# Optimization experiments

Measured on AMD Instinct MI355X. Metric: run time of the kernel, lower is better.

Reference implementation:

```python
import jax, jax.numpy as jnp
import numpy as np

N, Q, D = 8, 900, 256
HB, WB = 200, 200
L, NH, P = 6, 8, 4
HD = D // NH
FF = 512
NCLS, NBOX = 10, 8
ODIM = NCLS + NBOX
THRESH = 0.5
OFFSET_SCALE = 1.0
SCALE = 1.0 / float(np.sqrt(HD))


def _ln(x, g, b, eps=1e-5):
    m = jnp.mean(x, axis=-1, keepdims=True)
    v = jnp.mean((x - m) ** 2, axis=-1, keepdims=True)
    return (x - m) * jax.lax.rsqrt(v + eps) * g + b


def _mha(x, Wq, bq, Wk, bk, Wv, bv, Wo, bo):
    q = (x @ Wq + bq).reshape(N, Q, NH, HD)
    k = (x @ Wk + bk).reshape(N, Q, NH, HD)
    v = (x @ Wv + bv).reshape(N, Q, NH, HD)
    att = jax.nn.softmax(jnp.einsum('bqhd,bkhd->bhqk', q, k) * SCALE, axis=-1)
    o = jnp.einsum('bhqk,bkhd->bqhd', att, v).reshape(N, Q, D)
    return o @ Wo + bo


def _deform(q, ref, bev, dv_W, dv_b, off_W, off_b, aw_W, aw_b, do_W, do_b):
    # value projection of BEV map: (N, HW, D) -> (N, NH, HW, HD)
    val = (bev @ dv_W + dv_b).reshape(N, HB * WB, NH, HD).transpose(0, 2, 1, 3)
    off = (q @ off_W + off_b).reshape(N, Q, NH, P, 2)
    aw = jax.nn.softmax((q @ aw_W + aw_b).reshape(N, Q, NH, P), axis=-1)
    # ref: (N,Q,1,2) pixel coords -> broadcast to (N,Q,NH,P,2)
    loc = ref[:, :, :, None, :] + off * OFFSET_SCALE
    x = jnp.clip(loc[..., 0], 0.0, WB - 1.0)
    y = jnp.clip(loc[..., 1], 0.0, HB - 1.0)
    x0 = jnp.floor(x)
    y0 = jnp.floor(y)
    x1 = jnp.minimum(x0 + 1.0, WB - 1.0)
    y1 = jnp.minimum(y0 + 1.0, HB - 1.0)
    wx = (x - x0).transpose(0, 2, 1, 3)[..., None]  # (N,NH,Q,P,1)
    wy = (y - y0).transpose(0, 2, 1, 3)[..., None]

    def gather(ix, iy):
        idx = (iy * WB + ix).astype(jnp.int32)               # (N,Q,NH,P)
        idx = idx.transpose(0, 2, 1, 3).reshape(N, NH, Q * P, 1)
        g = jnp.take_along_axis(val, idx, axis=2)            # (N,NH,Q*P,HD)
        return g.reshape(N, NH, Q, P, HD)

    samp = (gather(x0, y0) * (1 - wx) * (1 - wy)
            + gather(x1, y0) * wx * (1 - wy)
            + gather(x0, y1) * (1 - wx) * wy
            + gather(x1, y1) * wx * wy)                      # (N,NH,Q,P,HD)
    awt = aw.transpose(0, 2, 1, 3)                           # (N,NH,Q,P)
    out = jnp.einsum('bhqp,bhqpd->bqhd', awt, samp).reshape(N, Q, D)
    return out @ do_W + do_b


def _ref_points():
    # n_sample=Q points evenly spread over the HBxWB grid, pixel coords, unnormalized
    idx = jnp.round(jnp.linspace(0.0, HB * WB - 1.0, Q)).astype(jnp.int32)
    x = (idx % WB).astype(jnp.float32)
    y = (idx // WB).astype(jnp.float32)
    rp = jnp.stack([x, y], axis=-1)                          # (Q,2)
    return jnp.broadcast_to(rp[None, :, None, :], (N, Q, 1, 2))


def _det(x, W1, b1, W2, b2):
    h = jax.nn.relu(x @ W1 + b1)
    o = h @ W2 + b2
    return jnp.concatenate([jax.nn.sigmoid(o[..., :NCLS]), o[..., NCLS:]], axis=-1)


def setup_inputs() -> dict:
    key = jax.random.key(0)
    ks = iter(jax.random.split(key, 48))

    def w(shape, s=0.02):
        return jax.random.normal(next(ks), shape, jnp.float32) * s

    inp = {
        'bev_features': jax.random.normal(next(ks), (N, HB * WB, D), jnp.float32),
        'pos_emb': w((Q, D), 1.0),
        'Wq': w((L, D, D)), 'bq': jnp.zeros((L, D), jnp.float32),
        'Wk': w((L, D, D)), 'bk': jnp.zeros((L, D), jnp.float32),
        'Wv': w((L, D, D)), 'bv': jnp.zeros((L, D), jnp.float32),
        'Wo': w((L, D, D)), 'bo': jnp.zeros((L, D), jnp.float32),
        'ln1_g': jnp.ones((L, D), jnp.float32), 'ln1_b': jnp.zeros((L, D), jnp.float32),
        'ln2_g': jnp.ones((L, D), jnp.float32), 'ln2_b': jnp.zeros((L, D), jnp.float32),
        'ln3_g': jnp.ones((L, D), jnp.float32), 'ln3_b': jnp.zeros((L, D), jnp.float32),
        'dv_W': w((L, D, D)), 'dv_b': jnp.zeros((L, D), jnp.float32),
        'off_W': w((L, D, NH * P * 2), 0.01), 'off_b': jnp.zeros((L, NH * P * 2), jnp.float32),
        'aw_W': w((L, D, NH * P), 0.01), 'aw_b': jnp.zeros((L, NH * P), jnp.float32),
        'do_W': w((L, D, D)), 'do_b': jnp.zeros((L, D), jnp.float32),
        'f1_W': w((L, D, FF)), 'f1_b': jnp.zeros((L, FF), jnp.float32),
        'f2_W': w((L, FF, D)), 'f2_b': jnp.zeros((L, D), jnp.float32),
        'det_W1': w((D, D)), 'det_b1': jnp.zeros((D,), jnp.float32),
        'det_W2': w((D, ODIM)), 'det_b2': jnp.zeros((ODIM,), jnp.float32),
    }
    return inp


def reference(bev_features, pos_emb, Wq, bq, Wk, bk, Wv, bv, Wo, bo,
              ln1_g, ln1_b, ln2_g, ln2_b, ln3_g, ln3_b,
              dv_W, dv_b, off_W, off_b, aw_W, aw_b, do_W, do_b,
              f1_W, f1_b, f2_W, f2_b, det_W1, det_b1, det_W2, det_b2):
    queries = jnp.broadcast_to(pos_emb[None], (N, Q, D))
    ref = _ref_points()
    output = queries
    layer_results = []
    for i in range(L):
        x = output + queries
        a = _mha(x, Wq[i], bq[i], Wk[i], bk[i], Wv[i], bv[i], Wo[i], bo[i])
        x2 = _ln(x + a, ln1_g[i], ln1_b[i])
        d = _deform(x2, ref, bev_features, dv_W[i], dv_b[i], off_W[i], off_b[i],
                    aw_W[i], aw_b[i], do_W[i], do_b[i])
        x3 = _ln(x2 + d, ln2_g[i], ln2_b[i])
        f = jax.nn.relu(x3 @ f1_W[i] + f1_b[i]) @ f2_W[i] + f2_b[i]
        output = _ln(x3 + f, ln3_g[i], ln3_b[i])
        layer_results.append(_det(output, det_W1, det_b1, det_W2, det_b2))
    layer_results = jnp.stack(layer_results, axis=0)   # (L,N,Q,ODIM)
    detections = layer_results[-1]
    track_mask = detections[..., 0] >= THRESH
    return output, detections, track_mask, layer_results
```

## Files before the change

kernel.cpp:

```cpp
#include <hip/hip_runtime.h>
#include <hip/hip_bf16.h>
#include <math.h>

#define N 8
#define Q 900
#define D 256
#define HB 200
#define WB 200
#define L 6
#define NH 8
#define P 4
#define HD 32
#define FF 512
#define NCLS 10
#define ODIM 18
#define HW (HB*WB)
#define NQ (N*Q)
#define NQD (NQ*D)
#define QD (Q*D)
#define SCALE 0.17677669529663687f

typedef __attribute__((ext_vector_type(4))) float f32x4;
typedef __attribute__((ext_vector_type(8))) short short8v;

__device__ __forceinline__ short bf16_of(float f) {
  __hip_bfloat16 h = __float2bfloat16(f);
  return __builtin_bit_cast(short, h);
}

#define TM 64
#define TN 64
#define KC 128

template <int ACT>
__global__ __launch_bounds__(256) void gemm_kernel(
    const float* __restrict__ A, const float* __restrict__ B,
    const float* __restrict__ bias, float* __restrict__ C,
    int M, int K, int Nc) {
  __shared__ float AsT[KC][TM + 4];
  __shared__ float Bs[KC][TN + 4];
  const int tid = threadIdx.x;
  const int tx = tid & 15, ty = tid >> 4;
  const int m0 = blockIdx.x * TM, n0 = blockIdx.y * TN;

  float c[4][4] = {};

  for (int kc = 0; kc < K; kc += KC) {
    {
      int r = tid >> 2;
      int gr = m0 + r;
      int kb = (tid & 3) * 32;
#pragma unroll
      for (int q = 0; q < 8; ++q) {
        int k = kb + q * 4;
        float4 av = make_float4(0.f, 0.f, 0.f, 0.f);
        if (gr < M) av = *(const float4*)(A + (size_t)gr * K + kc + k);
        AsT[k + 0][r] = av.x; AsT[k + 1][r] = av.y;
        AsT[k + 2][r] = av.z; AsT[k + 3][r] = av.w;
      }
    }
    {
#pragma unroll
      for (int i = 0; i < 8; ++i) {
        int idx = i * 256 + tid;
        int kr = idx >> 4;
        int c4 = (idx & 15) * 4;
        *(float4*)&Bs[kr][c4] = *(const float4*)(B + (size_t)(kc + kr) * Nc + n0 + c4);
      }
    }
    __syncthreads();
#pragma unroll 8
    for (int kk = 0; kk < KC; ++kk) {
      float4 av = *(const float4*)&AsT[kk][ty * 4];
      float4 bv = *(const float4*)&Bs[kk][tx * 4];
      c[0][0] += av.x * bv.x; c[0][1] += av.x * bv.y; c[0][2] += av.x * bv.z; c[0][3] += av.x * bv.w;
      c[1][0] += av.y * bv.x; c[1][1] += av.y * bv.y; c[1][2] += av.y * bv.z; c[1][3] += av.y * bv.w;
      c[2][0] += av.z * bv.x; c[2][1] += av.z * bv.y; c[2][2] += av.z * bv.z; c[2][3] += av.z * bv.w;
      c[3][0] += av.w * bv.x; c[3][1] += av.w * bv.y; c[3][2] += av.w * bv.z; c[3][3] += av.w * bv.w;
    }
    __syncthreads();
  }

#pragma unroll
  for (int i = 0; i < 4; ++i) {
    int row = m0 + ty * 4 + i;
    if (row >= M) continue;
#pragma unroll
    for (int j = 0; j < 4; ++j) {
      int col = n0 + tx * 4 + j;
      float v = c[i][j] + bias[col];
      if (ACT == 1) v = fmaxf(v, 0.f);
      C[(size_t)row * Nc + col] = v;
    }
  }
}

__global__ __launch_bounds__(256) void gemm_qkv_kernel(
    const float* __restrict__ outp, const float* __restrict__ pos,
    const float* __restrict__ Wq, const float* __restrict__ bq,
    const float* __restrict__ Wk, const float* __restrict__ bk,
    const float* __restrict__ Wv, const float* __restrict__ bv,
    float* __restrict__ Oq, float* __restrict__ Ok, float* __restrict__ Ov) {
  __shared__ float AsT[KC][TM + 4];
  __shared__ float Bs[KC][TN + 4];
  const int tid = threadIdx.x;
  const int tx = tid & 15, ty = tid >> 4;
  const int m0 = blockIdx.x * TM;
  const int wsel = blockIdx.y >> 2;
  const int n0 = (blockIdx.y & 3) * TN;
  const float* B = (wsel == 0) ? Wq : (wsel == 1) ? Wk : Wv;
  const float* bias = (wsel == 0) ? bq : (wsel == 1) ? bk : bv;
  float* C = (wsel == 0) ? Oq : (wsel == 1) ? Ok : Ov;

  float c[4][4] = {};

  for (int kc = 0; kc < D; kc += KC) {
    {
      int r = tid >> 2;
      int gr = m0 + r;
      int kb = (tid & 3) * 32;
      const float* ar = outp + (size_t)gr * D + kc;
      const float* pr = pos + (size_t)(gr % Q) * D + kc;
#pragma unroll
      for (int q = 0; q < 8; ++q) {
        int k = kb + q * 4;
        float4 av = make_float4(0.f, 0.f, 0.f, 0.f);
        if (gr < NQ) {
          float4 ov = *(const float4*)(ar + k);
          float4 pv = *(const float4*)(pr + k);
          av.x = ov.x + pv.x; av.y = ov.y + pv.y; av.z = ov.z + pv.z; av.w = ov.w + pv.w;
        }
        AsT[k + 0][r] = av.x; AsT[k + 1][r] = av.y;
        AsT[k + 2][r] = av.z; AsT[k + 3][r] = av.w;
      }
    }
    {
#pragma unroll
      for (int i = 0; i < 8; ++i) {
        int idx = i * 256 + tid;
        int kr = idx >> 4;
        int c4 = (idx & 15) * 4;
        *(float4*)&Bs[kr][c4] = *(const float4*)(B + (size_t)(kc + kr) * D + n0 + c4);
      }
    }
    __syncthreads();
#pragma unroll 8
    for (int kk = 0; kk < KC; ++kk) {
      float4 av = *(const float4*)&AsT[kk][ty * 4];
      float4 bv4 = *(const float4*)&Bs[kk][tx * 4];
      c[0][0] += av.x * bv4.x; c[0][1] += av.x * bv4.y; c[0][2] += av.x * bv4.z; c[0][3] += av.x * bv4.w;
      c[1][0] += av.y * bv4.x; c[1][1] += av.y * bv4.y; c[1][2] += av.y * bv4.z; c[1][3] += av.y * bv4.w;
      c[2][0] += av.z * bv4.x; c[2][1] += av.z * bv4.y; c[2][2] += av.z * bv4.z; c[2][3] += av.z * bv4.w;
      c[3][0] += av.w * bv4.x; c[3][1] += av.w * bv4.y; c[3][2] += av.w * bv4.z; c[3][3] += av.w * bv4.w;
    }
    __syncthreads();
  }

#pragma unroll
  for (int i = 0; i < 4; ++i) {
    int row = m0 + ty * 4 + i;
    if (row >= NQ) continue;
#pragma unroll
    for (int j = 0; j < 4; ++j) {
      int col = n0 + tx * 4 + j;
      C[(size_t)row * D + col] = c[i][j] + bias[col];
    }
  }
}

#define TMT 64
#define TKT 16
template <int ACT>
__global__ __launch_bounds__(256) void gemm_thin_kernel(
    const float* __restrict__ A, const float* __restrict__ B,
    const float* __restrict__ bias, float* __restrict__ C,
    int M, int K, int Nc) {
  __shared__ float AsT[TKT][TMT + 4];
  __shared__ float Bs[TKT][16 + 2];
  const int tid = threadIdx.x;
  const int tx = tid & 15, ty = tid >> 4;
  const int m0 = blockIdx.x * TMT, n0 = blockIdx.y * 16;

  float c[4] = {};

  for (int kt = 0; kt < K; kt += TKT) {
    {
      int r = tid >> 2;
      int cb = (tid & 3) * 4;
      int gr = m0 + r;
      float4 av = make_float4(0.f, 0.f, 0.f, 0.f);
      if (gr < M) av = *(const float4*)(A + (size_t)gr * K + kt + cb);
      AsT[cb + 0][r] = av.x;
      AsT[cb + 1][r] = av.y;
      AsT[cb + 2][r] = av.z;
      AsT[cb + 3][r] = av.w;
    }
    {
      int r = tid >> 4;
      int cc = tid & 15;
      int gc = n0 + cc;
      Bs[r][cc] = (gc < Nc) ? B[(size_t)(kt + r) * Nc + gc] : 0.f;
    }
    __syncthreads();
#pragma unroll
    for (int kk = 0; kk < TKT; ++kk) {
      float4 av = *(const float4*)&AsT[kk][ty * 4];
      float bv = Bs[kk][tx];
      c[0] += av.x * bv; c[1] += av.y * bv; c[2] += av.z * bv; c[3] += av.w * bv;
    }
    __syncthreads();
  }

  int col = n0 + tx;
  if (col < Nc) {
    float bs = bias[col];
#pragma unroll
    for (int i = 0; i < 4; ++i) {
      int row = m0 + ty * 4 + i;
      if (row < M) {
        float v = c[i] + bs;
        if (ACT == 2 && col < NCLS) v = 1.f / (1.f + expf(-v));
        C[(size_t)row * Nc + col] = v;
      }
    }
  }
}

__global__ __launch_bounds__(256) void gemm_offaw_kernel(
    const float* __restrict__ A,
    const float* __restrict__ offW, const float* __restrict__ offb,
    const float* __restrict__ awW, const float* __restrict__ awb,
    float* __restrict__ offC, float* __restrict__ awC) {
  __shared__ float AsT[TKT][TMT + 4];
  __shared__ float Bs[TKT][16 + 2];
  const int tid = threadIdx.x;
  const int tx = tid & 15, ty = tid >> 4;
  const int m0 = blockIdx.x * TMT;
  const bool isOff = blockIdx.y < 4;
  const int n0 = isOff ? blockIdx.y * 16 : (blockIdx.y - 4) * 16;
  const int Nc = isOff ? 64 : 32;
  const float* B = isOff ? offW : awW;
  const float* bias = isOff ? offb : awb;
  float* C = isOff ? offC : awC;

  float c[4] = {};

  for (int kt = 0; kt < D; kt += TKT) {
    {
      int r = tid >> 2;
      int cb = (tid & 3) * 4;
      int gr = m0 + r;
      float4 av = make_float4(0.f, 0.f, 0.f, 0.f);
      if (gr < NQ) av = *(const float4*)(A + (size_t)gr * D + kt + cb);
      AsT[cb + 0][r] = av.x;
      AsT[cb + 1][r] = av.y;
      AsT[cb + 2][r] = av.z;
      AsT[cb + 3][r] = av.w;
    }
    {
      int r = tid >> 4;
      int cc = tid & 15;
      Bs[r][cc] = B[(size_t)(kt + r) * Nc + n0 + cc];
    }
    __syncthreads();
#pragma unroll
    for (int kk = 0; kk < TKT; ++kk) {
      float4 av = *(const float4*)&AsT[kk][ty * 4];
      float bv = Bs[kk][tx];
      c[0] += av.x * bv; c[1] += av.y * bv; c[2] += av.z * bv; c[3] += av.w * bv;
    }
    __syncthreads();
  }

  int col = n0 + tx;
  float bs = bias[col];
#pragma unroll
  for (int i = 0; i < 4; ++i) {
    int row = m0 + ty * 4 + i;
    if (row < NQ) C[(size_t)row * Nc + col] = c[i] + bs;
  }
}

__global__ __launch_bounds__(256) void attn_kernel(
    const float* __restrict__ qg, const float* __restrict__ kg,
    const float* __restrict__ vg, float* __restrict__ og) {
  const int n = blockIdx.z, h = blockIdx.y;
  const int wv = threadIdx.x >> 6;
  const int lane = threadIdx.x & 63;
  const int g = lane >> 4;
  const int c = lane & 15;
  const int q0 = blockIdx.x * 64 + wv * 16;

  const float* qb = qg + (size_t)n * Q * D + h * HD;
  const float* kb = kg + (size_t)n * Q * D + h * HD;
  const float* vb = vg + (size_t)n * Q * D + h * HD;

  short8v qf = {};
  {
    int qr = q0 + c;
    if (qr < Q) {
      const float* qp = qb + (size_t)qr * D + g * 8;
#pragma unroll
      for (int j = 0; j < 8; ++j) qf[j] = bf16_of(qp[j]);
    }
  }

  const float SC2 = SCALE * 1.4426950408889634f;
  float m2 = -1e30f, l = 0.f;
  f32x4 acc0 = {0.f, 0.f, 0.f, 0.f}, acc1 = {0.f, 0.f, 0.f, 0.f};

  for (int kt0 = 0; kt0 < Q; kt0 += 64) {
    float s[16];
#pragma unroll
    for (int t = 0; t < 4; ++t) {
      short8v kf = {};
      int kr = kt0 + t * 16 + c;
      if (kr < Q) {
        const float* kp = kb + (size_t)kr * D + g * 8;
#pragma unroll
        for (int j = 0; j < 8; ++j) kf[j] = bf16_of(kp[j]);
      }
      f32x4 d = __builtin_amdgcn_mfma_f32_16x16x32_bf16(kf, qf, (f32x4){0.f, 0.f, 0.f, 0.f}, 0, 0, 0);
#pragma unroll
      for (int r = 0; r < 4; ++r) s[t * 4 + r] = d[r];
    }
#pragma unroll
    for (int t = 0; t < 4; ++t)
#pragma unroll
      for (int r = 0; r < 4; ++r) {
        int key = kt0 + t * 16 + g * 4 + r;
        s[t * 4 + r] = (key < Q) ? s[t * 4 + r] * SC2 : -1e30f;
      }
    float tm = s[0];
#pragma unroll
    for (int j = 1; j < 16; ++j) tm = fmaxf(tm, s[j]);
    tm = fmaxf(tm, __shfl_xor(tm, 16));
    tm = fmaxf(tm, __shfl_xor(tm, 32));
    float m2n = fmaxf(m2, tm);
    float corr = exp2f(m2 - m2n);
    m2 = m2n;
    float ps = 0.f;
#pragma unroll
    for (int j = 0; j < 16; ++j) { s[j] = exp2f(s[j] - m2); ps += s[j]; }
    ps += __shfl_xor(ps, 16);
    ps += __shfl_xor(ps, 32);
    l = l * corr + ps;
    float cr0 = __shfl(corr, g * 4 + 0);
    float cr1 = __shfl(corr, g * 4 + 1);
    float cr2 = __shfl(corr, g * 4 + 2);
    float cr3 = __shfl(corr, g * 4 + 3);
    acc0[0] *= cr0; acc0[1] *= cr1; acc0[2] *= cr2; acc0[3] *= cr3;
    acc1[0] *= cr0; acc1[1] *= cr1; acc1[2] *= cr2; acc1[3] *= cr3;

#pragma unroll
    for (int pr = 0; pr < 2; ++pr) {
      short8v pa, v0 = {}, v1 = {};
#pragma unroll
      for (int j = 0; j < 8; ++j) pa[j] = bf16_of(s[pr * 8 + j]);
#pragma unroll
      for (int j = 0; j < 8; ++j) {
        int key = kt0 + (pr * 2 + (j >> 2)) * 16 + g * 4 + (j & 3);
        if (key < Q) {
          const float* vp = vb + (size_t)key * D;
          v0[j] = bf16_of(vp[c]);
          v1[j] = bf16_of(vp[c + 16]);
        }
      }
      acc0 = __builtin_amdgcn_mfma_f32_16x16x32_bf16(pa, v0, acc0, 0, 0, 0);
      acc1 = __builtin_amdgcn_mfma_f32_16x16x32_bf16(pa, v1, acc1, 0, 0, 0);
    }
  }

  float inv = 1.f / l;
  float iv[4];
#pragma unroll
  for (int r = 0; r < 4; ++r) iv[r] = __shfl(inv, g * 4 + r);
#pragma unroll
  for (int r = 0; r < 4; ++r) {
    int qr = q0 + g * 4 + r;
    if (qr < Q) {
      float* op = og + (size_t)(n * Q + qr) * D + h * HD;
      op[c] = acc0[r] * iv[r];
      op[c + 16] = acc1[r] * iv[r];
    }
  }
}

__global__ __launch_bounds__(256) void ln_add_kernel(
    const float* __restrict__ A, const float* __restrict__ Bp,
    const float* __restrict__ g, const float* __restrict__ b,
    float* __restrict__ out) {
  const int wave = threadIdx.x >> 6;
  const int lane = threadIdx.x & 63;
  const int row = blockIdx.x * 4 + wave;
  const size_t base = (size_t)row * D + lane * 4;
  float4 a4 = *(const float4*)(A + base);
  float4 b4 = *(const float4*)(Bp + base);
  float v0 = a4.x + b4.x, v1 = a4.y + b4.y, v2 = a4.z + b4.z, v3 = a4.w + b4.w;
  float sum = v0 + v1 + v2 + v3;
#pragma unroll
  for (int off = 1; off < 64; off <<= 1) sum += __shfl_xor(sum, off);
  float mean = sum * (1.f / D);
  float d0 = v0 - mean, d1 = v1 - mean, d2 = v2 - mean, d3 = v3 - mean;
  float vsum = d0 * d0 + d1 * d1 + d2 * d2 + d3 * d3;
#pragma unroll
  for (int off = 1; off < 64; off <<= 1) vsum += __shfl_xor(vsum, off);
  float inv_std = 1.0f / sqrtf(vsum * (1.f / D) + 1e-5f);
  float4 g4 = *(const float4*)(g + lane * 4);
  float4 bb4 = *(const float4*)(b + lane * 4);
  float4 o4;
  o4.x = d0 * inv_std * g4.x + bb4.x;
  o4.y = d1 * inv_std * g4.y + bb4.y;
  o4.z = d2 * inv_std * g4.z + bb4.z;
  o4.w = d3 * inv_std * g4.w + bb4.w;
  *(float4*)(out + base) = o4;
}

__global__ __launch_bounds__(256) void ln_add3_kernel(
    const float* __restrict__ A, const float* __restrict__ pos,
    const float* __restrict__ Bp,
    const float* __restrict__ g, const float* __restrict__ b,
    float* __restrict__ out) {
  const int wave = threadIdx.x >> 6;
  const int lane = threadIdx.x & 63;
  const int row = blockIdx.x * 4 + wave;
  const size_t base = (size_t)row * D + lane * 4;
  const size_t pbase = (size_t)(row % Q) * D + lane * 4;
  float4 a4 = *(const float4*)(A + base);
  float4 p4 = *(const float4*)(pos + pbase);
  float4 b4 = *(const float4*)(Bp + base);
  float x0 = a4.x + p4.x, x1 = a4.y + p4.y, x2 = a4.z + p4.z, x3 = a4.w + p4.w;
  float v0 = x0 + b4.x, v1 = x1 + b4.y, v2 = x2 + b4.z, v3 = x3 + b4.w;
  float sum = v0 + v1 + v2 + v3;
#pragma unroll
  for (int off = 1; off < 64; off <<= 1) sum += __shfl_xor(sum, off);
  float mean = sum * (1.f / D);
  float d0 = v0 - mean, d1 = v1 - mean, d2 = v2 - mean, d3 = v3 - mean;
  float vsum = d0 * d0 + d1 * d1 + d2 * d2 + d3 * d3;
#pragma unroll
  for (int off = 1; off < 64; off <<= 1) vsum += __shfl_xor(vsum, off);
  float inv_std = 1.0f / sqrtf(vsum * (1.f / D) + 1e-5f);
  float4 g4 = *(const float4*)(g + lane * 4);
  float4 bb4 = *(const float4*)(b + lane * 4);
  float4 o4;
  o4.x = d0 * inv_std * g4.x + bb4.x;
  o4.y = d1 * inv_std * g4.y + bb4.y;
  o4.z = d2 * inv_std * g4.z + bb4.z;
  o4.w = d3 * inv_std * g4.w + bb4.w;
  *(float4*)(out + base) = o4;
}

__global__ __launch_bounds__(256) void deform_kernel(
    const float* __restrict__ bev, const float* __restrict__ offB,
    const float* __restrict__ awB, const float* __restrict__ dvW,
    const float* __restrict__ dvb, float* __restrict__ dtmp) {
  const int bq0 = blockIdx.x * 4;
  const int n = bq0 / Q;
  const int t = threadIdx.x;

  __shared__ float aw_s[4][NH * P];
  __shared__ int   idx_s[4][NH * P * 4];
  __shared__ float w_s[4][NH * P * 4];
  __shared__ float agg_s[4][NH][D];
  __shared__ float red_s[4][4][D];

  if (t < 128) {
    int qq = t >> 5, e = t & 31;
    int bq = bq0 + qq;
    int qi = bq - n * Q;
    float tq = __fmul_rn((float)qi, 44.492767333984375f);
    int ir = (int)rintf(tq);
    float rx = (float)(ir % WB);
    float ry = (float)(ir / WB);
    float ox = offB[(size_t)bq * 64 + e * 2 + 0];
    float oy = offB[(size_t)bq * 64 + e * 2 + 1];
    float lx = fminf(fmaxf(rx + ox, 0.f), (float)(WB - 1));
    float ly = fminf(fmaxf(ry + oy, 0.f), (float)(HB - 1));
    float x0 = floorf(lx), y0 = floorf(ly);
    float x1 = fminf(x0 + 1.f, (float)(WB - 1));
    float y1 = fminf(y0 + 1.f, (float)(HB - 1));
    float wx = lx - x0, wy = ly - y0;
    int b4 = e * 4;
    idx_s[qq][b4 + 0] = (int)y0 * WB + (int)x0; w_s[qq][b4 + 0] = (1.f - wx) * (1.f - wy);
    idx_s[qq][b4 + 1] = (int)y0 * WB + (int)x1; w_s[qq][b4 + 1] = wx * (1.f - wy);
    idx_s[qq][b4 + 2] = (int)y1 * WB + (int)x0; w_s[qq][b4 + 2] = (1.f - wx) * wy;
    idx_s[qq][b4 + 3] = (int)y1 * WB + (int)x1; w_s[qq][b4 + 3] = wx * wy;
  } else if (t < 160) {
    int idx = t - 128;
    int qq = idx >> 3, hh = idx & 7;
    const float* ap = awB + (size_t)(bq0 + qq) * 32 + hh * P;
    float l0 = ap[0], l1 = ap[1], l2 = ap[2], l3 = ap[3];
    float mx = fmaxf(fmaxf(l0, l1), fmaxf(l2, l3));
    float e0 = expf(l0 - mx), e1 = expf(l1 - mx), e2 = expf(l2 - mx), e3 = expf(l3 - mx);
    float inv = 1.f / (e0 + e1 + e2 + e3);
    aw_s[qq][hh * P + 0] = e0 * inv; aw_s[qq][hh * P + 1] = e1 * inv;
    aw_s[qq][hh * P + 2] = e2 * inv; aw_s[qq][hh * P + 3] = e3 * inv;
  }
  __syncthreads();

  {
    const float* bevn = bev + (size_t)n * HW * D;
    const int wv = t >> 6, lane = t & 63;
    const int c4 = lane * 4;
#pragma unroll
    for (int u = 0; u < 8; ++u) {
      int pid = wv + u * 4;
      int qq = pid >> 3, h = pid & 7;
      f32x4 acc = {0.f, 0.f, 0.f, 0.f};
#pragma unroll
      for (int p = 0; p < P; ++p) {
        int e = h * P + p;
        float aw = aw_s[qq][e];
        const int* ix = &idx_s[qq][e * 4];
        const float* wsp = &w_s[qq][e * 4];
        float4 g0 = *(const float4*)(bevn + (size_t)ix[0] * D + c4);
        float4 g1 = *(const float4*)(bevn + (size_t)ix[1] * D + c4);
        float4 g2 = *(const float4*)(bevn + (size_t)ix[2] * D + c4);
        float4 g3 = *(const float4*)(bevn + (size_t)ix[3] * D + c4);
        acc[0] += aw * (wsp[0] * g0.x + wsp[1] * g1.x + wsp[2] * g2.x + wsp[3] * g3.x);
        acc[1] += aw * (wsp[0] * g0.y + wsp[1] * g1.y + wsp[2] * g2.y + wsp[3] * g3.y);
        acc[2] += aw * (wsp[0] * g0.z + wsp[1] * g1.z + wsp[2] * g2.z + wsp[3] * g3.z);
        acc[3] += aw * (wsp[0] * g0.w + wsp[1] * g1.w + wsp[2] * g2.w + wsp[3] * g3.w);
      }
      *(f32x4*)&agg_s[qq][h][c4] = acc;
    }
  }
  __syncthreads();

  {
    const int chunk = t >> 6;
    const int col4 = t & 63;
    const int tt0 = col4 * 4;
    const int h = tt0 >> 5;
    f32x4 p[4] = {{0.f,0.f,0.f,0.f},{0.f,0.f,0.f,0.f},{0.f,0.f,0.f,0.f},{0.f,0.f,0.f,0.f}};
#pragma unroll 4
    for (int dd4 = 0; dd4 < 64; dd4 += 4) {
      int dd = chunk * 64 + dd4;
      float4 w0 = *(const float4*)(dvW + (size_t)(dd + 0) * D + tt0);
      float4 w1 = *(const float4*)(dvW + (size_t)(dd + 1) * D + tt0);
      float4 w2 = *(const float4*)(dvW + (size_t)(dd + 2) * D + tt0);
      float4 w3 = *(const float4*)(dvW + (size_t)(dd + 3) * D + tt0);
#pragma unroll
      for (int qq = 0; qq < 4; ++qq) {
        float4 a = *(const float4*)&agg_s[qq][h][dd];
        p[qq][0] += a.x * w0.x + a.y * w1.x + a.z * w2.x + a.w * w3.x;
        p[qq][1] += a.x * w0.y + a.y * w1.y + a.z * w2.y + a.w * w3.y;
        p[qq][2] += a.x * w0.z + a.y * w1.z + a.z * w2.z + a.w * w3.z;
        p[qq][3] += a.x * w0.w + a.y * w1.w + a.z * w2.w + a.w * w3.w;
      }
    }
#pragma unroll
    for (int qq = 0; qq < 4; ++qq) *(f32x4*)&red_s[qq][chunk][tt0] = p[qq];
  }
  __syncthreads();
  {
    float bs = dvb[t];
#pragma unroll
    for (int qq = 0; qq < 4; ++qq) {
      dtmp[(size_t)(bq0 + qq) * D + t] =
          bs + red_s[qq][0][t] + red_s[qq][1][t] + red_s[qq][2][t] + red_s[qq][3][t];
    }
  }
}

__global__ void bcast_q_kernel(const float* __restrict__ pos, float* __restrict__ out) {
  for (size_t i = (size_t)blockIdx.x * blockDim.x + threadIdx.x; i < (size_t)NQD;
       i += (size_t)gridDim.x * blockDim.x)
    out[i] = pos[i % QD];
}
__global__ void finalize_kernel(const float* __restrict__ lr5, float* __restrict__ det,
                                float* __restrict__ mask) {
  int i = blockIdx.x * blockDim.x + threadIdx.x;
  if (i < NQ * ODIM) det[i] = lr5[i];
  if (i < NQ) mask[i] = (lr5[(size_t)i * ODIM] >= 0.5f) ? 1.0f : 0.0f;
}

extern "C" void kernel_launch(void* const* d_in, const int* in_sizes, int n_in,
                              void* d_out, int out_size, void* d_ws, size_t ws_size,
                              hipStream_t stream) {
  const float* bev  = (const float*)d_in[0];
  const float* pos  = (const float*)d_in[1];
  const float* Wq   = (const float*)d_in[2];  const float* bq  = (const float*)d_in[3];
  const float* Wk   = (const float*)d_in[4];  const float* bk  = (const float*)d_in[5];
  const float* Wv   = (const float*)d_in[6];  const float* bv  = (const float*)d_in[7];
  const float* Wo   = (const float*)d_in[8];  const float* bo  = (const float*)d_in[9];
  const float* ln1g = (const float*)d_in[10]; const float* ln1b = (const float*)d_in[11];
  const float* ln2g = (const float*)d_in[12]; const float* ln2b = (const float*)d_in[13];
  const float* ln3g = (const float*)d_in[14]; const float* ln3b = (const float*)d_in[15];
  const float* dvW  = (const float*)d_in[16]; const float* dvb = (const float*)d_in[17];
  const float* offW = (const float*)d_in[18]; const float* offb = (const float*)d_in[19];
  const float* awW  = (const float*)d_in[20]; const float* awb = (const float*)d_in[21];
  const float* doW  = (const float*)d_in[22]; const float* dob = (const float*)d_in[23];
  const float* f1W  = (const float*)d_in[24]; const float* f1b = (const float*)d_in[25];
  const float* f2W  = (const float*)d_in[26]; const float* f2b = (const float*)d_in[27];
  const float* dW1  = (const float*)d_in[28]; const float* db1 = (const float*)d_in[29];
  const float* dW2  = (const float*)d_in[30]; const float* db2 = (const float*)d_in[31];

  float* w = (float*)d_ws;
  float* b0 = w + 0 * (size_t)NQD;
  float* b1 = w + 1 * (size_t)NQD;
  float* b2 = w + 2 * (size_t)NQD;
  float* b3 = w + 3 * (size_t)NQD;
  float* ffh = b1;
  float* offB = b0;
  float* awB  = b0 + (size_t)NQ * 64;

  float* out_output = (float*)d_out;
  float* out_det    = out_output + (size_t)NQD;
  float* out_mask   = out_det + (size_t)NQ * ODIM;
  float* out_lr     = out_mask + (size_t)NQ;

  const dim3 blk256(256);
  const dim3 qkvGrid((NQ + TM - 1) / TM, 12);
  const dim3 gemmGridD((NQ + TM - 1) / TM, D / TN);
  const dim3 gemmGridFF((NQ + TM - 1) / TM, FF / TN);
  const dim3 offawGrid((NQ + TMT - 1) / TMT, 6);
  const dim3 thinGridDet((NQ + TMT - 1) / TMT, 2);
  const dim3 attnGrid((Q + 63) / 64, NH, N);
  const dim3 lnGrid(NQ / 4);
  const dim3 defGrid(NQ / 4);
  const int ewGrid = 1024;

  bcast_q_kernel<<<ewGrid, blk256, 0, stream>>>(pos, out_output);

  for (int i = 0; i < L; ++i) {
    const size_t wDD = (size_t)i * D * D;
    gemm_qkv_kernel<<<qkvGrid, blk256, 0, stream>>>(out_output, pos,
        Wq + wDD, bq + (size_t)i * D, Wk + wDD, bk + (size_t)i * D,
        Wv + wDD, bv + (size_t)i * D, b1, b2, b3);
    attn_kernel<<<attnGrid, blk256, 0, stream>>>(b1, b2, b3, b0);
    gemm_kernel<0><<<gemmGridD, blk256, 0, stream>>>(b0, Wo + wDD, bo + (size_t)i * D, b1, NQ, D, D);
    ln_add3_kernel<<<lnGrid, blk256, 0, stream>>>(out_output, pos, b1,
        ln1g + (size_t)i * D, ln1b + (size_t)i * D, b2);
    gemm_offaw_kernel<<<offawGrid, blk256, 0, stream>>>(b2,
        offW + (size_t)i * D * 64, offb + (size_t)i * 64,
        awW + (size_t)i * D * 32, awb + (size_t)i * 32, offB, awB);
    deform_kernel<<<defGrid, blk256, 0, stream>>>(bev, offB, awB, dvW + wDD, dvb + (size_t)i * D, b3);
    gemm_kernel<0><<<gemmGridD, blk256, 0, stream>>>(b3, doW + wDD, dob + (size_t)i * D, b1, NQ, D, D);
    ln_add_kernel<<<lnGrid, blk256, 0, stream>>>(b2, b1, ln2g + (size_t)i * D, ln2b + (size_t)i * D, b0);
    gemm_kernel<1><<<gemmGridFF, blk256, 0, stream>>>(b0, f1W + (size_t)i * D * FF, f1b + (size_t)i * FF, ffh, NQ, D, FF);
    gemm_kernel<0><<<gemmGridD, blk256, 0, stream>>>(ffh, f2W + (size_t)i * FF * D, f2b + (size_t)i * D, b3, NQ, FF, D);
    ln_add_kernel<<<lnGrid, blk256, 0, stream>>>(b0, b3, ln3g + (size_t)i * D, ln3b + (size_t)i * D, out_output);
    gemm_kernel<1><<<gemmGridD, blk256, 0, stream>>>(out_output, dW1, db1, b1, NQ, D, D);
    gemm_thin_kernel<2><<<thinGridDet, blk256, 0, stream>>>(b1, dW2, db2, out_lr + (size_t)i * NQ * ODIM, NQ, D, ODIM);
  }

  finalize_kernel<<<(NQ * ODIM + 255) / 256, blk256, 0, stream>>>(out_lr + (size_t)(L - 1) * NQ * ODIM,
                                                                  out_det, out_mask);
}
```

Before: 2.522 ms.

## Store QKV projections as bf16 and enlarge K-chunk in thin GEMMs

```diff
diff --git a/kernel.cpp b/kernel.cpp
--- a/kernel.cpp
+++ b/kernel.cpp
@@ -100,7 +100,8 @@
     const float* __restrict__ Wq, const float* __restrict__ bq,
     const float* __restrict__ Wk, const float* __restrict__ bk,
     const float* __restrict__ Wv, const float* __restrict__ bv,
-    float* __restrict__ Oq, float* __restrict__ Ok, float* __restrict__ Ov) {
+    unsigned short* __restrict__ Oq, unsigned short* __restrict__ Ok,
+    unsigned short* __restrict__ Ov) {
   __shared__ float AsT[KC][TM + 4];
   __shared__ float Bs[KC][TN + 4];
   const int tid = threadIdx.x;
@@ -110,7 +111,7 @@
   const int n0 = (blockIdx.y & 3) * TN;
   const float* B = (wsel == 0) ? Wq : (wsel == 1) ? Wk : Wv;
   const float* bias = (wsel == 0) ? bq : (wsel == 1) ? bk : bv;
-  float* C = (wsel == 0) ? Oq : (wsel == 1) ? Ok : Ov;
+  unsigned short* C = (wsel == 0) ? Oq : (wsel == 1) ? Ok : Ov;
 
   float c[4][4] = {};
 
@@ -160,50 +161,56 @@
   for (int i = 0; i < 4; ++i) {
     int row = m0 + ty * 4 + i;
     if (row >= NQ) continue;
-#pragma unroll
-    for (int j = 0; j < 4; ++j) {
-      int col = n0 + tx * 4 + j;
-      C[(size_t)row * D + col] = c[i][j] + bias[col];
-    }
+    ushort4 o4;
+    o4.x = (unsigned short)bf16_of(c[i][0] + bias[n0 + tx * 4 + 0]);
+    o4.y = (unsigned short)bf16_of(c[i][1] + bias[n0 + tx * 4 + 1]);
+    o4.z = (unsigned short)bf16_of(c[i][2] + bias[n0 + tx * 4 + 2]);
+    o4.w = (unsigned short)bf16_of(c[i][3] + bias[n0 + tx * 4 + 3]);
+    *(ushort4*)(C + (size_t)row * D + n0 + tx * 4) = o4;
   }
 }
 
 #define TMT 64
-#define TKT 16
 template <int ACT>
 __global__ __launch_bounds__(256) void gemm_thin_kernel(
     const float* __restrict__ A, const float* __restrict__ B,
     const float* __restrict__ bias, float* __restrict__ C,
     int M, int K, int Nc) {
-  __shared__ float AsT[TKT][TMT + 4];
-  __shared__ float Bs[TKT][16 + 2];
+  __shared__ float AsT[KC][TMT + 4];
+  __shared__ float Bs[KC][16 + 2];
   const int tid = threadIdx.x;
   const int tx = tid & 15, ty = tid >> 4;
   const int m0 = blockIdx.x * TMT, n0 = blockIdx.y * 16;
 
   float c[4] = {};
 
-  for (int kt = 0; kt < K; kt += TKT) {
+  for (int kc = 0; kc < K; kc += KC) {
     {
       int r = tid >> 2;
-      int cb = (tid & 3) * 4;
       int gr = m0 + r;
-      float4 av = make_float4(0.f, 0.f, 0.f, 0.f);
-      if (gr < M) av = *(const float4*)(A + (size_t)gr * K + kt + cb);
-      AsT[cb + 0][r] = av.x;
-      AsT[cb + 1][r] = av.y;
-      AsT[cb + 2][r] = av.z;
-      AsT[cb + 3][r] = av.w;
-    }
-    {
-      int r = tid >> 4;
-      int cc = tid & 15;
-      int gc = n0 + cc;
-      Bs[r][cc] = (gc < Nc) ? B[(size_t)(kt + r) * Nc + gc] : 0.f;
-    }
-    __syncthreads();
-#pragma unroll
-    for (int kk = 0; kk < TKT; ++kk) {
+      int kb = (tid & 3) * 32;
+#pragma unroll
+      for (int q = 0; q < 8; ++q) {
+        int k = kb + q * 4;
+        float4 av = make_float4(0.f, 0.f, 0.f, 0.f);
+        if (gr < M) av = *(const float4*)(A + (size_t)gr * K + kc + k);
+        AsT[k + 0][r] = av.x; AsT[k + 1][r] = av.y;
+        AsT[k + 2][r] = av.z; AsT[k + 3][r] = av.w;
+      }
+    }
+    {
+#pragma unroll
+      for (int i = 0; i < 8; ++i) {
+        int idx = i * 256 + tid;
+        int kr = idx >> 4;
+        int cc = idx & 15;
+        int gc = n0 + cc;
+        Bs[kr][cc] = (gc < Nc) ? B[(size_t)(kc + kr) * Nc + gc] : 0.f;
+      }
+    }
+    __syncthreads();
+#pragma unroll 8
+    for (int kk = 0; kk < KC; ++kk) {
       float4 av = *(const float4*)&AsT[kk][ty * 4];
       float bv = Bs[kk][tx];
       c[0] += av.x * bv; c[1] += av.y * bv; c[2] += av.z * bv; c[3] += av.w * bv;
@@ -231,8 +238,8 @@
     const float* __restrict__ offW, const float* __restrict__ offb,
     const float* __restrict__ awW, const float* __restrict__ awb,
     float* __restrict__ offC, float* __restrict__ awC) {
-  __shared__ float AsT[TKT][TMT + 4];
-  __shared__ float Bs[TKT][16 + 2];
+  __shared__ float AsT[KC][TMT + 4];
+  __shared__ float Bs[KC][16 + 2];
   const int tid = threadIdx.x;
   const int tx = tid & 15, ty = tid >> 4;
   const int m0 = blockIdx.x * TMT;
@@ -245,26 +252,32 @@
 
   float c[4] = {};
 
-  for (int kt = 0; kt < D; kt += TKT) {
+  for (int kc = 0; kc < D; kc += KC) {
     {
       int r = tid >> 2;
-      int cb = (tid & 3) * 4;
       int gr = m0 + r;
-      float4 av = make_float4(0.f, 0.f, 0.f, 0.f);
-      if (gr < NQ) av = *(const float4*)(A + (size_t)gr * D + kt + cb);
-      AsT[cb + 0][r] = av.x;
-      AsT[cb + 1][r] = av.y;
-      AsT[cb + 2][r] = av.z;
-      AsT[cb + 3][r] = av.w;
-    }
-    {
-      int r = tid >> 4;
-      int cc = tid & 15;
-      Bs[r][cc] = B[(size_t)(kt + r) * Nc + n0 + cc];
-    }
-    __syncthreads();
-#pragma unroll
-    for (int kk = 0; kk < TKT; ++kk) {
+      int kb = (tid & 3) * 32;
+#pragma unroll
+      for (int q = 0; q < 8; ++q) {
+        int k = kb + q * 4;
+        float4 av = make_float4(0.f, 0.f, 0.f, 0.f);
+        if (gr < NQ) av = *(const float4*)(A + (size_t)gr * D + kc + k);
+        AsT[k + 0][r] = av.x; AsT[k + 1][r] = av.y;
+        AsT[k + 2][r] = av.z; AsT[k + 3][r] = av.w;
+      }
+    }
+    {
+#pragma unroll
+      for (int i = 0; i < 8; ++i) {
+        int idx = i * 256 + tid;
+        int kr = idx >> 4;
+        int cc = idx & 15;
+        Bs[kr][cc] = B[(size_t)(kc + kr) * Nc + n0 + cc];
+      }
+    }
+    __syncthreads();
+#pragma unroll 8
+    for (int kk = 0; kk < KC; ++kk) {
       float4 av = *(const float4*)&AsT[kk][ty * 4];
       float bv = Bs[kk][tx];
       c[0] += av.x * bv; c[1] += av.y * bv; c[2] += av.z * bv; c[3] += av.w * bv;
@@ -282,8 +295,8 @@
 }
 
 __global__ __launch_bounds__(256) void attn_kernel(
-    const float* __restrict__ qg, const float* __restrict__ kg,
-    const float* __restrict__ vg, float* __restrict__ og) {
+    const unsigned short* __restrict__ qg, const unsigned short* __restrict__ kg,
+    const unsigned short* __restrict__ vg, float* __restrict__ og) {
   const int n = blockIdx.z, h = blockIdx.y;
   const int wv = threadIdx.x >> 6;
   const int lane = threadIdx.x & 63;
@@ -291,18 +304,14 @@
   const int c = lane & 15;
   const int q0 = blockIdx.x * 64 + wv * 16;
 
-  const float* qb = qg + (size_t)n * Q * D + h * HD;
-  const float* kb = kg + (size_t)n * Q * D + h * HD;
-  const float* vb = vg + (size_t)n * Q * D + h * HD;
+  const unsigned short* qb = qg + (size_t)n * Q * D + h * HD;
+  const unsigned short* kb = kg + (size_t)n * Q * D + h * HD;
+  const unsigned short* vb = vg + (size_t)n * Q * D + h * HD;
 
   short8v qf = {};
   {
     int qr = q0 + c;
-    if (qr < Q) {
-      const float* qp = qb + (size_t)qr * D + g * 8;
-#pragma unroll
-      for (int j = 0; j < 8; ++j) qf[j] = bf16_of(qp[j]);
-    }
+    if (qr < Q) qf = *(const short8v*)(qb + (size_t)qr * D + g * 8);
   }
 
   const float SC2 = SCALE * 1.4426950408889634f;
@@ -315,11 +324,7 @@
     for (int t = 0; t < 4; ++t) {
       short8v kf = {};
       int kr = kt0 + t * 16 + c;
-      if (kr < Q) {
-        const float* kp = kb + (size_t)kr * D + g * 8;
-#pragma unroll
-        for (int j = 0; j < 8; ++j) kf[j] = bf16_of(kp[j]);
-      }
+      if (kr < Q) kf = *(const short8v*)(kb + (size_t)kr * D + g * 8);
       f32x4 d = __builtin_amdgcn_mfma_f32_16x16x32_bf16(kf, qf, (f32x4){0.f, 0.f, 0.f, 0.f}, 0, 0, 0);
 #pragma unroll
       for (int r = 0; r < 4; ++r) s[t * 4 + r] = d[r];
@@ -361,9 +366,9 @@
       for (int j = 0; j < 8; ++j) {
         int key = kt0 + (pr * 2 + (j >> 2)) * 16 + g * 4 + (j & 3);
         if (key < Q) {
-          const float* vp = vb + (size_t)key * D;
-          v0[j] = bf16_of(vp[c]);
-          v1[j] = bf16_of(vp[c + 16]);
+          const unsigned short* vp = vb + (size_t)key * D;
+          v0[j] = (short)vp[c];
+          v1[j] = (short)vp[c + 16];
         }
       }
       acc0 = __builtin_amdgcn_mfma_f32_16x16x32_bf16(pa, v0, acc0, 0, 0, 0);
@@ -604,6 +609,9 @@
   float* ffh = b1;
   float* offB = b0;
   float* awB  = b0 + (size_t)NQ * 64;
+  unsigned short* qb16 = (unsigned short*)b1;
+  unsigned short* kb16 = (unsigned short*)b1 + NQD;
+  unsigned short* vb16 = (unsigned short*)b2;
 
   float* out_output = (float*)d_out;
   float* out_det    = out_output + (size_t)NQD;
@@ -627,8 +635,8 @@
     const size_t wDD = (size_t)i * D * D;
     gemm_qkv_kernel<<<qkvGrid, blk256, 0, stream>>>(out_output, pos,
         Wq + wDD, bq + (size_t)i * D, Wk + wDD, bk + (size_t)i * D,
-        Wv + wDD, bv + (size_t)i * D, b1, b2, b3);
-    attn_kernel<<<attnGrid, blk256, 0, stream>>>(b1, b2, b3, b0);
+        Wv + wDD, bv + (size_t)i * D, qb16, kb16, vb16);
+    attn_kernel<<<attnGrid, blk256, 0, stream>>>(qb16, kb16, vb16, b0);
     gemm_kernel<0><<<gemmGridD, blk256, 0, stream>>>(b0, Wo + wDD, bo + (size_t)i * D, b1, NQ, D, D);
     ln_add3_kernel<<<lnGrid, blk256, 0, stream>>>(out_output, pos, b1,
         ln1g + (size_t)i * D, ln1b + (size_t)i * D, b2);
```

Result: faster. 2.418 ms, median of 2 (-4.1%).
